# Kernel tuning notes

Measured on AMD Instinct MI355X. Metric: run time of the kernel, lower is better.

The kernel has to match this reference:

```python
import jax, jax.numpy as jnp
import numpy as np

EMBED = 1024
HEADS = 16
HEAD_DIM = EMBED // HEADS


def setup_inputs() -> dict:
    key = jax.random.key(0)
    ks = jax.random.split(key, 12)
    B, S = 2, 2048
    inp = {
        'v': jax.random.normal(ks[0], (B, S, EMBED), jnp.float32),
        'k': jax.random.normal(ks[1], (B, S, EMBED), jnp.float32),
        'q': jax.random.normal(ks[2], (B, S, EMBED), jnp.float32),
        'mask': jnp.ones((B, 1, S, S), dtype=bool),
        'Wv': jax.random.normal(ks[3], (EMBED, EMBED), jnp.float32) * 0.02,
        'bv': jax.random.normal(ks[4], (EMBED,), jnp.float32) * 0.02,
        'Wk': jax.random.normal(ks[5], (EMBED, EMBED), jnp.float32) * 0.02,
        'bk': jax.random.normal(ks[6], (EMBED,), jnp.float32) * 0.02,
        'Wq': jax.random.normal(ks[7], (EMBED, EMBED), jnp.float32) * 0.02,
        'bq': jax.random.normal(ks[8], (EMBED,), jnp.float32) * 0.02,
        'Wo': jax.random.normal(ks[9], (EMBED, EMBED), jnp.float32) * 0.02,
        'bo': jax.random.normal(ks[10], (EMBED,), jnp.float32) * 0.02,
    }
    return inp


def reference(v, k, q, mask, Wv, bv, Wk, bk, Wq, bq, Wo, bo):
    N, q_len, _ = q.shape
    k_len = k.shape[1]
    # linear projections (torch Linear: x @ W.T + b)
    vh = (v @ Wv.T + bv).reshape(N, -1, HEADS, HEAD_DIM)
    kh = (k @ Wk.T + bk).reshape(N, k_len, HEADS, HEAD_DIM)
    qh = (q @ Wq.T + bq).reshape(N, q_len, HEADS, HEAD_DIM)
    # scores [N, H, q, k]
    energy = jnp.einsum('nqhd,nkhd->nhqk', qh, kh)
    # NOTE: original masks BEFORE dividing by sqrt(embed_size)
    energy = jnp.where(mask, energy, jnp.float32(-1e20))
    attention = jax.nn.softmax(energy / jnp.sqrt(jnp.float32(EMBED)), axis=3)
    out = jnp.einsum('nhqk,nkhd->nqhd', attention, vh).reshape(N, q_len, EMBED)
    return out @ Wo.T + bo
```

## Files before the change

kernel.cpp:

```cpp
#include <hip/hip_runtime.h>
#include <cstdint>
#include <cstddef>


typedef uint16_t u16;
typedef uint32_t u32;
typedef unsigned long long u64;
using bf16x8 = __attribute__((ext_vector_type(8))) __bf16;
using bf16x2 = __attribute__((ext_vector_type(2))) __bf16;
using f32x4  = __attribute__((ext_vector_type(4))) float;
using f32x16 = __attribute__((ext_vector_type(16))) float;
using u16x8  = __attribute__((ext_vector_type(8))) uint16_t;
using u16x4  = __attribute__((ext_vector_type(4))) uint16_t;
using u32x4  = __attribute__((ext_vector_type(4))) uint32_t;

#define S_LEN 2048
#define EMB   1024
#define NHEAD 16
#define HDIM  64
#define BATCH 2
#define MROWS (BATCH * S_LEN)
#define NBITW (BATCH * S_LEN * (S_LEN / 64))

__device__ __forceinline__ u16 f2bf(float f) {
  uint32_t u = __float_as_uint(f);
  u += 0x7FFFu + ((u >> 16) & 1u);
  return (u16)(u >> 16);
}

__device__ __forceinline__ float fexp2(float x) {
#if __has_builtin(__builtin_amdgcn_exp2f)
  return __builtin_amdgcn_exp2f(x);
#else
  return exp2f(x);
#endif
}

__device__ __forceinline__ u32 packbf(float a, float b) {
  bf16x2 v = { (__bf16)a, (__bf16)b };
  return __builtin_bit_cast(u32, v);
}

__device__ __forceinline__ void plswap(u32& a, u32& b) {
  asm volatile("v_permlane32_swap_b32 %0, %1" : "+v"(a), "+v"(b));
}

__device__ __forceinline__ float xhalf_sum(float x) {
  u32 a = __builtin_bit_cast(u32, x), b;
  asm volatile("v_mov_b32 %0, %1" : "=v"(b) : "v"(a));
  asm volatile("v_permlane32_swap_b32 %0, %1" : "+v"(a), "+v"(b));
  return __builtin_bit_cast(float, a) + __builtin_bit_cast(float, b);
}

__device__ __forceinline__ float tree16(const f32x16& v) {
  float t0 = v[0] + v[1], t1 = v[2] + v[3], t2 = v[4] + v[5], t3 = v[6] + v[7];
  float t4 = v[8] + v[9], t5 = v[10] + v[11], t6 = v[12] + v[13], t7 = v[14] + v[15];
  float u0 = t0 + t1, u1 = t2 + t3, u2 = t4 + t5, u3 = t6 + t7;
  return (u0 + u1) + (u2 + u3);
}

__device__ __forceinline__ void async16(void* lds, const void* g) {
  __builtin_amdgcn_global_load_lds(
      (const __attribute__((address_space(1))) void*)g,
      (__attribute__((address_space(3))) void*)lds, 16, 0, 0);
}

__global__ __launch_bounds__(256) void mask_compact(const uint32_t* __restrict__ m,
                                                    u64* __restrict__ bits) {
  const int i = blockIdx.x * 256 + threadIdx.x;
  if (i >= NBITW) return;
  const bool bytew = (m[0] == 0x01010101u);
  u64 b = 0;
  if (bytew) {
    const uint32_t* src = m + (size_t)i * 16;
#pragma unroll
    for (int w = 0; w < 16; ++w) {
      const uint32_t v = src[w];
#pragma unroll
      for (int j = 0; j < 4; ++j)
        b |= (u64)(((v >> (8 * j)) & 0xFFu) != 0u) << (w * 4 + j);
    }
  } else {
    const uint32_t* src = m + (size_t)i * 64;
#pragma unroll
    for (int j = 0; j < 64; ++j) b |= (u64)(src[j] != 0u) << j;
  }
  bits[i] = b;
}

struct ConvArgs {
  const float* src[7];
  u16* dst[7];
  int n4[7];
};

__global__ __launch_bounds__(256) void convert_bf16(ConvArgs a) {
  const int j = blockIdx.y;
  const float4* s = (const float4*)a.src[j];
  u16* d = a.dst[j];
  const int n4 = a.n4[j];
  for (int i = blockIdx.x * 256 + threadIdx.x; i < n4; i += gridDim.x * 256) {
    float4 v = s[i];
    u16x4 o = { f2bf(v.x), f2bf(v.y), f2bf(v.z), f2bf(v.w) };
    *(u16x4*)(d + (size_t)i * 4) = o;
  }
}

__device__ __forceinline__ void gemm_body_bk64(const u16* __restrict__ A,
                                               const u16* __restrict__ W,
                                               const float* __restrict__ bias,
                                               u16* __restrict__ C, float scale,
                                               int m0, int n0) {
  constexpr int K = 1024, N = 1024;
  __shared__ alignas(16) u16 As[128 * 64];
  __shared__ alignas(16) u16 Bs[128 * 64];
  const int t = threadIdx.x;
  const int wave = t >> 6, lane = t & 63;
  const int wr = wave >> 1, wc = wave & 1;
  f32x4 acc[4][4] = {};
  const int f = lane >> 3;
  const int soff = ((lane & 7) ^ f) * 8;
  const int srowp = wave * 8 + f;
  const int fr = lane & 15;
  const int q4 = lane >> 4;

  for (int kt = 0; kt < K; kt += 64) {
#pragma unroll
    for (int i = 0; i < 4; ++i)
      async16(As + i * 2048 + wave * 512,
              A + (size_t)(m0 + i * 32 + srowp) * K + kt + soff);
#pragma unroll
    for (int i = 0; i < 4; ++i)
      async16(Bs + i * 2048 + wave * 512,
              W + (size_t)(n0 + i * 32 + srowp) * K + kt + soff);
    __syncthreads();
#pragma unroll
    for (int kk = 0; kk < 2; ++kk) {
      bf16x8 af[4], bfr[4];
#pragma unroll
      for (int i = 0; i < 4; ++i) {
        const int row = wr * 64 + i * 16 + fr;
        af[i] = *(const bf16x8*)((const char*)As + row * 128 +
                                 (((q4 + kk * 4) ^ (row & 7)) << 4));
      }
#pragma unroll
      for (int i = 0; i < 4; ++i) {
        const int row = wc * 64 + i * 16 + fr;
        bfr[i] = *(const bf16x8*)((const char*)Bs + row * 128 +
                                  (((q4 + kk * 4) ^ (row & 7)) << 4));
      }
#pragma unroll
      for (int mi = 0; mi < 4; ++mi)
#pragma unroll
        for (int ni = 0; ni < 4; ++ni)
          acc[mi][ni] = __builtin_amdgcn_mfma_f32_16x16x32_bf16(
              af[mi], bfr[ni], acc[mi][ni], 0, 0, 0);
    }
    __syncthreads();
  }
  const int r0 = (lane >> 4) * 4;
#pragma unroll
  for (int mi = 0; mi < 4; ++mi) {
    const int rowb = m0 + wr * 64 + mi * 16 + r0;
#pragma unroll
    for (int ni = 0; ni < 4; ++ni) {
      const int col = n0 + wc * 64 + ni * 16 + fr;
      const float bv = bias[col];
#pragma unroll
      for (int r = 0; r < 4; ++r)
        C[(size_t)(rowb + r) * N + col] = f2bf((acc[mi][ni][r] + bv) * scale);
    }
  }
}

struct ProjArgs {
  const u16* A[3];
  const u16* W[3];
  const float* bias[3];
  u16* C[3];
  float scale[3];
};

__global__ __launch_bounds__(256) void gemm_proj3(ProjArgs p) {
  const int lin = blockIdx.x + 8 * blockIdx.y + 256 * blockIdx.z;
  const int logical = (lin & 7) * 96 + (lin >> 3);
  const int z = logical >> 8;
  const int rem = logical & 255;
  const int n0 = (rem & 7) * 128, m0 = (rem >> 3) * 128;
  gemm_body_bk64(p.A[z], p.W[z], p.bias[z], p.C[z], p.scale[z], m0, n0);
}

__global__ __launch_bounds__(256) void gemm_out(const u16* __restrict__ A,
                                                const u16* __restrict__ W,
                                                const float* __restrict__ bias,
                                                float* __restrict__ C) {
  constexpr int BM = 64, BN = 128, FM = 2, FN = 4;
  constexpr int K = 1024, N = 1024;
  __shared__ alignas(16) u16 As[BM * 32];
  __shared__ alignas(16) u16 Bs[BN * 32];
  const int t = threadIdx.x;
  const int wave = t >> 6, lane = t & 63;
  const int wr = wave >> 1, wc = wave & 1;
  const int lin = blockIdx.x + 8 * blockIdx.y;
  const int logical = (lin & 7) * 64 + (lin >> 3);
  const int m0 = (logical >> 3) * BM, n0 = (logical & 7) * BN;
  f32x4 acc[FM][FN] = {};
  const int srow = wave * 16 + (lane >> 2);
  const int soff = (lane & 3) * 8;
  const u16* gA = A + (size_t)(m0 + srow) * K + soff;
  const u16* gB = W + (size_t)(n0 + srow) * K + soff;
  u16* lA = As + wave * 512;
  u16* lB = Bs + wave * 512;
  const int fo = (lane >> 4) * 8;
  const int fr = lane & 15;

  for (int kt = 0; kt < K; kt += 32) {
    async16(lA, gA + kt);
#pragma unroll
    for (int a = 0; a < BN / 64; ++a)
      async16(lB + a * 2048, gB + (size_t)(a * 64) * K + kt);
    __syncthreads();
    bf16x8 af[FM], bfr[FN];
#pragma unroll
    for (int i = 0; i < FM; ++i)
      af[i] = *(const bf16x8*)(As + (wr * (FM * 16) + i * 16 + fr) * 32 + fo);
#pragma unroll
    for (int i = 0; i < FN; ++i)
      bfr[i] = *(const bf16x8*)(Bs + (wc * (FN * 16) + i * 16 + fr) * 32 + fo);
#pragma unroll
    for (int mi = 0; mi < FM; ++mi)
#pragma unroll
      for (int ni = 0; ni < FN; ++ni)
        acc[mi][ni] = __builtin_amdgcn_mfma_f32_16x16x32_bf16(af[mi], bfr[ni],
                                                              acc[mi][ni], 0, 0, 0);
    __syncthreads();
  }
  const int r0 = (lane >> 4) * 4;
#pragma unroll
  for (int mi = 0; mi < FM; ++mi) {
    const int rowb = m0 + wr * (FM * 16) + mi * 16 + r0;
#pragma unroll
    for (int ni = 0; ni < FN; ++ni) {
      const int col = n0 + wc * (FN * 16) + ni * 16 + fr;
      const float bv = bias[col];
#pragma unroll
      for (int r = 0; r < 4; ++r)
        C[(size_t)(rowb + r) * N + col] = acc[mi][ni][r] + bv;
    }
  }
}

__global__ __launch_bounds__(256, 2) void attn_fa(const u16* __restrict__ Qh,
                                                  const u16* __restrict__ Kh,
                                                  const u16* __restrict__ Vh,
                                                  const u64* __restrict__ mbits,
                                                  u16* __restrict__ O) {
  __shared__ alignas(16) u16 Kt[2][64 * 64];
  __shared__ alignas(16) u16 Vt[2][64 * 64];
  const int t = threadIdx.x, wave = t >> 6, lane = t & 63;
  const int lin = blockIdx.x + 16 * blockIdx.y;
  const int logical = (lin & 7) * 64 + (lin >> 3);
  const int wbx = logical & 15;
  const int wbh = logical >> 4;
  const int b = wbh >> 4, h = wbh & 15;
  const int ql = lane & 31;
  const int hi = lane >> 5;
  const int qrow = wbx * 128 + wave * 32 + ql;

  const u16* qbase = Qh + (size_t)(b * S_LEN + qrow) * EMB + h * HDIM + hi * 8;
  bf16x8 qf[4];
#pragma unroll
  for (int dk = 0; dk < 4; ++dk)
    qf[dk] = *(const bf16x8*)(qbase + dk * 16);

  const int srow = t >> 3;
  const int schunk = t & 7;
  const int fk0 = (srow + (srow >> 3)) & 7;
  const int fk1 = (srow + 32 + ((srow + 32) >> 3)) & 7;
  const u16* kbase = Kh + (size_t)(b * S_LEN) * EMB + h * HDIM;
  const u16* vbase = Vh + (size_t)(b * S_LEN) * EMB + h * HDIM;
  const int vdg = t & 7, vkp = t >> 3;
  const int vd0 = vdg * 8, vk0 = vkp * 2;
  const int vg_hi = (vkp >> 2) & 7, vg_lo = (vkp & 3) * 4;

  u16x8 va, vb;
  {
    async16(&Kt[0][0] + wave * 512,
            kbase + (size_t)srow * EMB + ((schunk ^ fk0) * 8));
    async16(&Kt[0][0] + 2048 + wave * 512,
            kbase + (size_t)(srow + 32) * EMB + ((schunk ^ fk1) * 8));
    const u16* vs = vbase + (size_t)vk0 * EMB + vd0;
    va = *(const u16x8*)vs;
    vb = *(const u16x8*)(vs + EMB);
  }
#pragma unroll
  for (int j = 0; j < 8; ++j) {
    const int d = vd0 + j;
    const int fd = (d + (d >> 3)) & 7;
    const u32 val = (u32)va[j] | ((u32)vb[j] << 16);
    *(u32*)((char*)&Vt[0][0] + (d * 128 + ((vg_hi ^ fd) << 4) + vg_lo)) = val;
  }
  __syncthreads();

  f32x16 o[2] = {};
  float lloc = 0.f;
  const u64* mword = mbits + (size_t)(b * S_LEN + qrow) * 32;

  for (int kt = 0; kt < 32; ++kt) {
    const int cur = kt & 1, nxt = cur ^ 1;
    if (kt < 31) {
      const int kvn = (kt + 1) * 64;
      async16(&Kt[nxt][0] + wave * 512,
              kbase + (size_t)(kvn + srow) * EMB + ((schunk ^ fk0) * 8));
      async16(&Kt[nxt][0] + 2048 + wave * 512,
              kbase + (size_t)(kvn + srow + 32) * EMB + ((schunk ^ fk1) * 8));
      const u16* vs = vbase + (size_t)(kvn + vk0) * EMB + vd0;
      va = *(const u16x8*)vs;
      vb = *(const u16x8*)(vs + EMB);
    }

    f32x16 s[2] = {};
    __builtin_amdgcn_s_setprio(1);
#pragma unroll
    for (int kb = 0; kb < 2; ++kb) {
      const int key = kb * 32 + ql;
      const int fkk = (key + (key >> 3)) & 7;
      const char* kRow = (const char*)&Kt[cur][0] + key * 128;
#pragma unroll
      for (int dk = 0; dk < 4; ++dk) {
        const bf16x8 kf =
            *(const bf16x8*)(kRow + (((dk * 2 + hi) ^ fkk) << 4));
        s[kb] = __builtin_amdgcn_mfma_f32_32x32x16_bf16(kf, qf[dk], s[kb], 0, 0, 0);
      }
    }
    __builtin_amdgcn_s_setprio(0);

    const u64 mw = mword[kt];
    if (!__all((int)(mw == ~0ull))) {
#pragma unroll
      for (int kb = 0; kb < 2; ++kb)
#pragma unroll
        for (int r = 0; r < 16; ++r) {
          const int key = 32 * kb + (r & 3) + 8 * (r >> 2) + 4 * hi;
          if (!((mw >> key) & 1ull)) s[kb][r] = -1.0e20f;
        }
    }

#pragma unroll
    for (int kb = 0; kb < 2; ++kb)
#pragma unroll
      for (int r = 0; r < 16; ++r) s[kb][r] = fexp2(s[kb][r]);
    lloc += tree16(s[0]) + tree16(s[1]);

    bf16x8 pf[4];
#pragma unroll
    for (int kb = 0; kb < 2; ++kb) {
      u32 w0 = packbf(s[kb][0], s[kb][1]);
      u32 w1 = packbf(s[kb][2], s[kb][3]);
      u32 w2 = packbf(s[kb][4], s[kb][5]);
      u32 w3 = packbf(s[kb][6], s[kb][7]);
      u32 w4 = packbf(s[kb][8], s[kb][9]);
      u32 w5 = packbf(s[kb][10], s[kb][11]);
      u32 w6 = packbf(s[kb][12], s[kb][13]);
      u32 w7 = packbf(s[kb][14], s[kb][15]);
      plswap(w0, w2);
      plswap(w1, w3);
      plswap(w4, w6);
      plswap(w5, w7);
      const u32x4 lo4 = {w0, w1, w2, w3};
      const u32x4 hi4 = {w4, w5, w6, w7};
      pf[kb * 2 + 0] = __builtin_bit_cast(bf16x8, lo4);
      pf[kb * 2 + 1] = __builtin_bit_cast(bf16x8, hi4);
    }

    __builtin_amdgcn_s_setprio(1);
#pragma unroll
    for (int dB = 0; dB < 2; ++dB) {
      const int d = dB * 32 + ql;
      const int fd = (d + (d >> 3)) & 7;
      const char* vRow = (const char*)&Vt[cur][0] + d * 128;
#pragma unroll
      for (int ks = 0; ks < 4; ++ks) {
        const bf16x8 vf =
            *(const bf16x8*)(vRow + (((ks * 2 + hi) ^ fd) << 4));
        o[dB] = __builtin_amdgcn_mfma_f32_32x32x16_bf16(vf, pf[ks], o[dB], 0, 0, 0);
      }
    }
    __builtin_amdgcn_s_setprio(0);

    if (kt < 31) {
#pragma unroll
      for (int j = 0; j < 8; ++j) {
        const int d = vd0 + j;
        const int fd = (d + (d >> 3)) & 7;
        const u32 val = (u32)va[j] | ((u32)vb[j] << 16);
        *(u32*)((char*)&Vt[nxt][0] + (d * 128 + ((vg_hi ^ fd) << 4) + vg_lo)) = val;
      }
    }
    __syncthreads();
  }

  const float inv = 1.0f / xhalf_sum(lloc);
  u16* ob = O + (size_t)(b * S_LEN + qrow) * EMB + h * HDIM;
#pragma unroll
  for (int dB = 0; dB < 2; ++dB)
#pragma unroll
    for (int rr = 0; rr < 4; ++rr) {
      u16x4 st;
#pragma unroll
      for (int m = 0; m < 4; ++m) st[m] = f2bf(o[dB][rr * 4 + m] * inv);
      *(u16x4*)(ob + dB * 32 + rr * 8 + hi * 4) = st;
    }
}

extern "C" void kernel_launch(void* const* d_in, const int* in_sizes, int n_in,
                              void* d_out, int out_size, void* d_ws, size_t ws_size,
                              hipStream_t stream) {
  const float* v_in = (const float*)d_in[0];
  const float* k_in = (const float*)d_in[1];
  const float* q_in = (const float*)d_in[2];
  const uint32_t* mask = (const uint32_t*)d_in[3];
  const float* Wv = (const float*)d_in[4];
  const float* bv = (const float*)d_in[5];
  const float* Wk = (const float*)d_in[6];
  const float* bk = (const float*)d_in[7];
  const float* Wq = (const float*)d_in[8];
  const float* bq = (const float*)d_in[9];
  const float* Wo = (const float*)d_in[10];
  const float* bo = (const float*)d_in[11];

  char* ws = (char*)d_ws;
  const size_t SZX = (size_t)MROWS * EMB * 2;
  const size_t SZW = (size_t)EMB * EMB * 2;
  u16* qh  = (u16*)(ws);
  u16* kh  = (u16*)(ws + SZX);
  u16* vh  = (u16*)(ws + 2 * SZX);
  u16* Obf = (u16*)(ws + 3 * SZX);
  u16* Wqb = (u16*)(ws + 4 * SZX);
  u16* Wkb = (u16*)(ws + 4 * SZX + SZW);
  u16* Wvb = (u16*)(ws + 4 * SZX + 2 * SZW);
  u16* Wob = (u16*)(ws + 4 * SZX + 3 * SZW);
  u16* qbf = (u16*)(ws + 4 * SZX + 4 * SZW);
  u16* kbf = (u16*)(ws + 5 * SZX + 4 * SZW);
  u16* vbf = (u16*)(ws + 6 * SZX + 4 * SZW);
  u64* mbits = (u64*)(ws + 7 * SZX + 4 * SZW);

  mask_compact<<<dim3(NBITW / 256), 256, 0, stream>>>(mask, mbits);

  ConvArgs ca;
  ca.src[0] = q_in; ca.dst[0] = qbf; ca.n4[0] = MROWS * EMB / 4;
  ca.src[1] = k_in; ca.dst[1] = kbf; ca.n4[1] = MROWS * EMB / 4;
  ca.src[2] = v_in; ca.dst[2] = vbf; ca.n4[2] = MROWS * EMB / 4;
  ca.src[3] = Wq;   ca.dst[3] = Wqb; ca.n4[3] = EMB * EMB / 4;
  ca.src[4] = Wk;   ca.dst[4] = Wkb; ca.n4[4] = EMB * EMB / 4;
  ca.src[5] = Wv;   ca.dst[5] = Wvb; ca.n4[5] = EMB * EMB / 4;
  ca.src[6] = Wo;   ca.dst[6] = Wob; ca.n4[6] = EMB * EMB / 4;
  convert_bf16<<<dim3(256, 7), 256, 0, stream>>>(ca);

  ProjArgs pa;
  const float qscale = 1.4426950408889634f / 32.0f;
  pa.A[0] = qbf; pa.W[0] = Wqb; pa.bias[0] = bq; pa.C[0] = qh; pa.scale[0] = qscale;
  pa.A[1] = kbf; pa.W[1] = Wkb; pa.bias[1] = bk; pa.C[1] = kh; pa.scale[1] = 1.0f;
  pa.A[2] = vbf; pa.W[2] = Wvb; pa.bias[2] = bv; pa.C[2] = vh; pa.scale[2] = 1.0f;
  gemm_proj3<<<dim3(8, 32, 3), 256, 0, stream>>>(pa);

  attn_fa<<<dim3(16, 32), 256, 0, stream>>>(qh, kh, vh, mbits, Obf);

  gemm_out<<<dim3(8, 64), 256, 0, stream>>>(Obf, Wob, bo, (float*)d_out);
}
```

Measured before the change: 133.8 us.

## Fuse fp32-to-bf16 activation conversion into projection GEMM A-tile load

The projection GEMM now reads the fp32 q/k/v activations directly, converts them to bf16 in registers and writes swizzled tiles to LDS. The next k-tile is prefetched into registers during the MFMA loop. This removes the separate conversion pass over the three activation tensors and their bf16 round trip through global memory. The price is that each projection block reads twice as many activation bytes (fp32), and the column tiles re-read them, adding register pressure and possibly lower occupancy in the GEMM.

```diff
diff --git a/kernel.cpp b/kernel.cpp
--- a/kernel.cpp
+++ b/kernel.cpp
@@ -89,16 +89,15 @@
 }
 
 struct ConvArgs {
-  const float* src[7];
-  u16* dst[7];
-  int n4[7];
+  const float* src[4];
+  u16* dst[4];
 };
 
 __global__ __launch_bounds__(256) void convert_bf16(ConvArgs a) {
   const int j = blockIdx.y;
   const float4* s = (const float4*)a.src[j];
   u16* d = a.dst[j];
-  const int n4 = a.n4[j];
+  const int n4 = EMB * EMB / 4;
   for (int i = blockIdx.x * 256 + threadIdx.x; i < n4; i += gridDim.x * 256) {
     float4 v = s[i];
     u16x4 o = { f2bf(v.x), f2bf(v.y), f2bf(v.z), f2bf(v.w) };
@@ -106,11 +105,11 @@
   }
 }
 
-__device__ __forceinline__ void gemm_body_bk64(const u16* __restrict__ A,
-                                               const u16* __restrict__ W,
-                                               const float* __restrict__ bias,
-                                               u16* __restrict__ C, float scale,
-                                               int m0, int n0) {
+__device__ __forceinline__ void gemm_fused_bk64(const float* __restrict__ A,
+                                                const u16* __restrict__ W,
+                                                const float* __restrict__ bias,
+                                                u16* __restrict__ C, float scale,
+                                                int m0, int n0) {
   constexpr int K = 1024, N = 1024;
   __shared__ alignas(16) u16 As[128 * 64];
   __shared__ alignas(16) u16 Bs[128 * 64];
@@ -121,14 +120,28 @@
   const int f = lane >> 3;
   const int soff = ((lane & 7) ^ f) * 8;
   const int srowp = wave * 8 + f;
+  const int ar = t >> 1, ah = t & 1;
+  const float* ga = A + (size_t)(m0 + ar) * K + ah * 32;
+  char* aw = (char*)As + ar * 128;
+  const int arf = ar & 7;
   const int fr = lane & 15;
   const int q4 = lane >> 4;
 
+  f32x4 va[8];
+#pragma unroll
+  for (int j = 0; j < 8; ++j) va[j] = *(const f32x4*)(ga + j * 4);
+
   for (int kt = 0; kt < K; kt += 64) {
-#pragma unroll
-    for (int i = 0; i < 4; ++i)
-      async16(As + i * 2048 + wave * 512,
-              A + (size_t)(m0 + i * 32 + srowp) * K + kt + soff);
+    {
+#pragma unroll
+      for (int j = 0; j < 4; ++j) {
+        const u16x8 w = { f2bf(va[2 * j][0]), f2bf(va[2 * j][1]),
+                          f2bf(va[2 * j][2]), f2bf(va[2 * j][3]),
+                          f2bf(va[2 * j + 1][0]), f2bf(va[2 * j + 1][1]),
+                          f2bf(va[2 * j + 1][2]), f2bf(va[2 * j + 1][3]) };
+        *(u16x8*)(aw + (((ah * 4 + j) ^ arf) << 4)) = w;
+      }
+    }
 #pragma unroll
     for (int i = 0; i < 4; ++i)
       async16(Bs + i * 2048 + wave * 512,
@@ -156,6 +169,11 @@
           acc[mi][ni] = __builtin_amdgcn_mfma_f32_16x16x32_bf16(
               af[mi], bfr[ni], acc[mi][ni], 0, 0, 0);
     }
+    if (kt + 64 < K) {
+#pragma unroll
+      for (int j = 0; j < 8; ++j)
+        va[j] = *(const f32x4*)(ga + kt + 64 + j * 4);
+    }
     __syncthreads();
   }
   const int r0 = (lane >> 4) * 4;
@@ -174,7 +192,7 @@
 }
 
 struct ProjArgs {
-  const u16* A[3];
+  const float* A[3];
   const u16* W[3];
   const float* bias[3];
   u16* C[3];
@@ -187,7 +205,7 @@
   const int z = logical >> 8;
   const int rem = logical & 255;
   const int n0 = (rem & 7) * 128, m0 = (rem >> 3) * 128;
-  gemm_body_bk64(p.A[z], p.W[z], p.bias[z], p.C[z], p.scale[z], m0, n0);
+  gemm_fused_bk64(p.A[z], p.W[z], p.bias[z], p.C[z], p.scale[z], m0, n0);
 }
 
 __global__ __launch_bounds__(256) void gemm_out(const u16* __restrict__ A,
@@ -440,28 +458,22 @@
   u16* Wkb = (u16*)(ws + 4 * SZX + SZW);
   u16* Wvb = (u16*)(ws + 4 * SZX + 2 * SZW);
   u16* Wob = (u16*)(ws + 4 * SZX + 3 * SZW);
-  u16* qbf = (u16*)(ws + 4 * SZX + 4 * SZW);
-  u16* kbf = (u16*)(ws + 5 * SZX + 4 * SZW);
-  u16* vbf = (u16*)(ws + 6 * SZX + 4 * SZW);
-  u64* mbits = (u64*)(ws + 7 * SZX + 4 * SZW);
+  u64* mbits = (u64*)(ws + 4 * SZX + 4 * SZW);
 
   mask_compact<<<dim3(NBITW / 256), 256, 0, stream>>>(mask, mbits);
 
   ConvArgs ca;
-  ca.src[0] = q_in; ca.dst[0] = qbf; ca.n4[0] = MROWS * EMB / 4;
-  ca.src[1] = k_in; ca.dst[1] = kbf; ca.n4[1] = MROWS * EMB / 4;
-  ca.src[2] = v_in; ca.dst[2] = vbf; ca.n4[2] = MROWS * EMB / 4;
-  ca.src[3] = Wq;   ca.dst[3] = Wqb; ca.n4[3] = EMB * EMB / 4;
-  ca.src[4] = Wk;   ca.dst[4] = Wkb; ca.n4[4] = EMB * EMB / 4;
-  ca.src[5] = Wv;   ca.dst[5] = Wvb; ca.n4[5] = EMB * EMB / 4;
-  ca.src[6] = Wo;   ca.dst[6] = Wob; ca.n4[6] = EMB * EMB / 4;
-  convert_bf16<<<dim3(256, 7), 256, 0, stream>>>(ca);
+  ca.src[0] = Wq; ca.dst[0] = Wqb;
+  ca.src[1] = Wk; ca.dst[1] = Wkb;
+  ca.src[2] = Wv; ca.dst[2] = Wvb;
+  ca.src[3] = Wo; ca.dst[3] = Wob;
+  convert_bf16<<<dim3(128, 4), 256, 0, stream>>>(ca);
 
   ProjArgs pa;
   const float qscale = 1.4426950408889634f / 32.0f;
-  pa.A[0] = qbf; pa.W[0] = Wqb; pa.bias[0] = bq; pa.C[0] = qh; pa.scale[0] = qscale;
-  pa.A[1] = kbf; pa.W[1] = Wkb; pa.bias[1] = bk; pa.C[1] = kh; pa.scale[1] = 1.0f;
-  pa.A[2] = vbf; pa.W[2] = Wvb; pa.bias[2] = bv; pa.C[2] = vh; pa.scale[2] = 1.0f;
+  pa.A[0] = q_in; pa.W[0] = Wqb; pa.bias[0] = bq; pa.C[0] = qh; pa.scale[0] = qscale;
+  pa.A[1] = k_in; pa.W[1] = Wkb; pa.bias[1] = bk; pa.C[1] = kh; pa.scale[1] = 1.0f;
+  pa.A[2] = v_in; pa.W[2] = Wvb; pa.bias[2] = bv; pa.C[2] = vh; pa.scale[2] = 1.0f;
   gemm_proj3<<<dim3(8, 32, 3), 256, 0, stream>>>(pa);
 
   attn_fa<<<dim3(16, 32), 256, 0, stream>>>(qh, kh, vh, mbits, Obf);
```

Result: slower. 170.7 us (+27.6%).
